# Performance work log

Measured on AMD Instinct MI355X. Metric: run time of the kernel, lower is better.

Reference implementation:

```python
import jax, jax.numpy as jnp
import numpy as np
import math

B, W, BINS, BANDS = 2, 2048, 1024, 8  # cropsize == W
HEAD = BINS // BANDS


def setup_inputs() -> dict:
    key = jax.random.key(0)
    ks = jax.random.split(key, 10)
    s = 1.0 / math.sqrt(BINS)
    return {
        "x": jax.random.normal(ks[0], (B, W, BINS), jnp.float32),
        "Wq": jax.random.normal(ks[1], (BINS, BINS), jnp.float32) * s,
        "bq": jax.random.normal(ks[2], (BINS,), jnp.float32) * s,
        "Wk": jax.random.normal(ks[3], (BINS, BINS), jnp.float32) * s,
        "bk": jax.random.normal(ks[4], (BINS,), jnp.float32) * s,
        "Wv": jax.random.normal(ks[5], (BINS, BINS), jnp.float32) * s,
        "bv": jax.random.normal(ks[6], (BINS,), jnp.float32) * s,
        "Wo": jax.random.normal(ks[7], (BINS, BINS), jnp.float32) * s,
        "bo": jax.random.normal(ks[8], (BINS,), jnp.float32) * s,
        "er": jax.random.normal(ks[9], (HEAD, W), jnp.float32) * s,  # [bins//num_bands, cropsize]
    }


def reference(x, Wq, bq, Wk, bk, Wv, bv, Wo, bo, er):
    b, w, h = x.shape
    n = BANDS
    # projections -> [b, n, w, head]
    q = (x @ Wq.T + bq).reshape(b, w, n, -1).transpose(0, 2, 1, 3)
    k = (x @ Wk.T + bk).reshape(b, w, n, -1).transpose(0, 2, 1, 3)
    v = (x @ Wv.T + bv).reshape(b, w, n, -1).transpose(0, 2, 1, 3)
    # relative position bias via skew trick: [b, n, w, cropsize]
    qer = jnp.einsum('bnwd,dc->bnwc', q, er)
    p = jnp.pad(qer, ((0, 0), (0, 0), (0, 0), (1, 0)))  # pad left of last dim
    p = jnp.swapaxes(p, 2, 3)[:, :, 1:, :]              # [b, n, w, w]
    a = (jnp.einsum('bnqd,bnkd->bnqk', q, k) + p) / math.sqrt(h)
    attn = jax.nn.softmax(a, axis=-1)
    ctx = jnp.einsum('bnqk,bnkd->bnqd', attn, v).transpose(0, 2, 1, 3).reshape(b, w, h)
    o = ctx @ Wo.T + bo
    return (o, a)
```

## Files before the change

kernel.cpp:

```cpp
#include <hip/hip_runtime.h>

typedef __attribute__((ext_vector_type(8))) __bf16 bf16x8;
typedef __attribute__((ext_vector_type(4))) float f32x4;

__device__ __forceinline__ unsigned short f2bf(float f) {
  __bf16 h = (__bf16)f;
  return __builtin_bit_cast(unsigned short, h);
}

__device__ __forceinline__ f32x4 mfma_bf16(bf16x8 a, bf16x8 b, f32x4 c) {
  return __builtin_amdgcn_mfma_f32_16x16x32_bf16(a, b, c, 0, 0, 0);
}

__device__ __forceinline__ void gload_lds16(const void* g, void* l) {
  __builtin_amdgcn_global_load_lds((const __attribute__((address_space(1))) void*)g,
                                   (__attribute__((address_space(3))) void*)l, 16, 0, 0);
}


__global__ void cvt_f32_bf16(const float* __restrict__ in, unsigned short* __restrict__ out, int n4) {
  int i = blockIdx.x * blockDim.x + threadIdx.x;
  if (i < n4) {
    float4 v = reinterpret_cast<const float4*>(in)[i];
    ushort4 o;
    o.x = f2bf(v.x); o.y = f2bf(v.y); o.z = f2bf(v.z); o.w = f2bf(v.w);
    reinterpret_cast<ushort4*>(out)[i] = o;
  }
}

__global__ void cvt4_f32_bf16(const float* __restrict__ a, const float* __restrict__ b,
                              const float* __restrict__ c, const float* __restrict__ d,
                              unsigned short* __restrict__ oa, unsigned short* __restrict__ ob,
                              unsigned short* __restrict__ oc, unsigned short* __restrict__ od) {
  int i = blockIdx.x * blockDim.x + threadIdx.x;
  int which = i >> 18, j = i & 262143;
  const float* src = (which == 0) ? a : (which == 1) ? b : (which == 2) ? c : d;
  unsigned short* dst = (which == 0) ? oa : (which == 1) ? ob : (which == 2) ? oc : od;
  float4 v = reinterpret_cast<const float4*>(src)[j];
  ushort4 o;
  o.x = f2bf(v.x); o.y = f2bf(v.y); o.z = f2bf(v.z); o.w = f2bf(v.w);
  reinterpret_cast<ushort4*>(dst)[j] = o;
}

__global__ void er_transpose(const float* __restrict__ er, unsigned short* __restrict__ ert) {
  __shared__ float t[32][33];
  int w0 = blockIdx.x * 32, d0 = blockIdx.y * 32;
  int tx = threadIdx.x, ty = threadIdx.y;
#pragma unroll
  for (int i = 0; i < 4; ++i)
    t[ty + i * 8][tx] = er[(size_t)(d0 + ty + i * 8) * 2048 + w0 + tx];
  __syncthreads();
#pragma unroll
  for (int i = 0; i < 4; ++i)
    ert[(size_t)(w0 + ty + i * 8) * 128 + d0 + tx] = f2bf(t[tx][ty + i * 8]);
}


__device__ __forceinline__ void gemm_tile(
    const unsigned short* __restrict__ A,
    const unsigned short* __restrict__ Bt,
    const float* __restrict__ bias,
    void* __restrict__ C,
    int mode, int i0, int j0,
    unsigned short* lds)
{
  unsigned short* Al = lds;
  unsigned short* Bl = lds + 4096;

  const int tid = threadIdx.x;
  const int lane = tid & 63, wid = tid >> 6;
  const int lr = lane & 15, lq = lane >> 4;
  const int wr = wid >> 1, wc = wid & 1;

  f32x4 acc[4][4] = {};

  const int srow = tid >> 2;
  const int scolb = (tid & 3) << 4;

  const char* Abase = (const char*)A + (size_t)(i0 + srow) * 2048 + scolb;
  const char* Bbase = (const char*)Bt + (size_t)(j0 + srow) * 2048 + scolb;

  for (int kt = 0; kt < 32; ++kt) {
    const int k0b = kt * 64;
    __syncthreads();
    gload_lds16(Abase + k0b,             (char*)Al + tid * 16);
    gload_lds16(Abase + k0b + 64 * 2048, (char*)Al + 4096 + tid * 16);
    gload_lds16(Bbase + k0b,             (char*)Bl + tid * 16);
    gload_lds16(Bbase + k0b + 64 * 2048, (char*)Bl + 4096 + tid * 16);
    __syncthreads();

    bf16x8 af[4], bfr[4];
#pragma unroll
    for (int m = 0; m < 4; ++m)
      af[m] = *(const bf16x8*)((const char*)Al + (wr * 64 + m * 16 + lr) * 64 + lq * 16);
#pragma unroll
    for (int n = 0; n < 4; ++n)
      bfr[n] = *(const bf16x8*)((const char*)Bl + (wc * 64 + n * 16 + lr) * 64 + lq * 16);
    __builtin_amdgcn_s_setprio(1);
#pragma unroll
    for (int m = 0; m < 4; ++m)
#pragma unroll
      for (int n = 0; n < 4; ++n)
        acc[m][n] = mfma_bf16(af[m], bfr[n], acc[m][n]);
    __builtin_amdgcn_s_setprio(0);
  }

  float bv[4];
#pragma unroll
  for (int n = 0; n < 4; ++n) bv[n] = bias[j0 + wc * 64 + n * 16 + lr];

  if (mode == 1) {
    __syncthreads();
#pragma unroll
    for (int m = 0; m < 4; ++m)
#pragma unroll
      for (int n = 0; n < 4; ++n)
#pragma unroll
        for (int r = 0; r < 4; ++r) {
          int il = wr * 64 + m * 16 + lq * 4 + r;
          int jl = wc * 64 + n * 16 + lr;
          lds[jl * 132 + il] = f2bf(acc[m][n][r] + bv[n]);
        }
    __syncthreads();
    const int b = i0 >> 11, w0 = i0 & 2047, bd = j0 >> 7;
    unsigned short* out = (unsigned short*)C;
    for (int idx = tid; idx < 16384; idx += 256) {
      int dl = idx >> 7, wl = idx & 127;
      out[(size_t)((b * 8 + bd) * 128 + dl) * 2048 + w0 + wl] = lds[dl * 132 + wl];
    }
  } else if (mode == 0) {
    unsigned short* out = (unsigned short*)C;
#pragma unroll
    for (int m = 0; m < 4; ++m)
#pragma unroll
      for (int n = 0; n < 4; ++n)
#pragma unroll
        for (int r = 0; r < 4; ++r) {
          int gi = i0 + wr * 64 + m * 16 + lq * 4 + r;
          int gj = j0 + wc * 64 + n * 16 + lr;
          out[(size_t)gi * 1024 + gj] = f2bf(acc[m][n][r] + bv[n]);
        }
  } else {
    float* out = (float*)C;
#pragma unroll
    for (int m = 0; m < 4; ++m)
#pragma unroll
      for (int n = 0; n < 4; ++n)
#pragma unroll
        for (int r = 0; r < 4; ++r) {
          int gi = i0 + wr * 64 + m * 16 + lq * 4 + r;
          int gj = j0 + wc * 64 + n * 16 + lr;
          out[(size_t)gi * 1024 + gj] = acc[m][n][r] + bv[n];
        }
  }
}

__global__ __launch_bounds__(256, 2) void gemm_qkv(
    const unsigned short* __restrict__ xb,
    const unsigned short* __restrict__ Wqb, const unsigned short* __restrict__ Wkb,
    const unsigned short* __restrict__ Wvb,
    const float* __restrict__ bq, const float* __restrict__ bk, const float* __restrict__ bv_,
    unsigned short* __restrict__ Qb, unsigned short* __restrict__ Kb,
    unsigned short* __restrict__ Vtb)
{
  __shared__ unsigned short lds[16896];
  const int which = blockIdx.y >> 3;
  const int i0 = blockIdx.x * 128, j0 = (blockIdx.y & 7) * 128;
  const unsigned short* Bt = (which == 0) ? Wqb : (which == 1) ? Wkb : Wvb;
  const float* bias = (which == 0) ? bq : (which == 1) ? bk : bv_;
  void* C = (which == 0) ? (void*)Qb : (which == 1) ? (void*)Kb : (void*)Vtb;
  gemm_tile(xb, Bt, bias, C, (which == 2) ? 1 : 0, i0, j0, lds);
}

__global__ __launch_bounds__(256, 2) void gemm_bt(
    const unsigned short* __restrict__ A,
    const unsigned short* __restrict__ Bt,
    const float* __restrict__ bias,
    void* __restrict__ C,
    int mode)
{
  __shared__ unsigned short lds[16896];
  gemm_tile(A, Bt, bias, C, mode, blockIdx.x * 128, blockIdx.y * 128, lds);
}


__global__ __launch_bounds__(512) void attn_fused(
    const unsigned short* __restrict__ Qb,
    const unsigned short* __restrict__ Kb,
    const unsigned short* __restrict__ Vt,
    const unsigned short* __restrict__ ErT,
    float* __restrict__ a_out,
    unsigned short* __restrict__ ctx)
{
  __shared__ __align__(16) char Klb[32768];
  __shared__ __align__(16) char Qlb[32768];
  __shared__ __align__(16) char Vlb[32768];
  __shared__ __align__(16) char Plb[32768];

  const int bb = blockIdx.x;
  const int bd = bb & 7, b = bb >> 3;
  const int qi0 = blockIdx.y * 128;
  const int tid = threadIdx.x, wid = tid >> 6, lane = tid & 63;
  const int lr = lane & 15, lq = lane >> 4;

  bf16x8 qf[4], ef[4];
  {
    const unsigned short* Qrow = Qb + (size_t)(b * 2048 + qi0 + wid * 16 + lr) * 1024 + bd * 128;
    const unsigned short* Erow = ErT + (size_t)(qi0 + wid * 16 + lr) * 128;
#pragma unroll
    for (int kk = 0; kk < 4; ++kk) {
      qf[kk] = *(const bf16x8*)(Qrow + kk * 32 + lq * 8);
      ef[kk] = *(const bf16x8*)(Erow + kk * 32 + lq * 8);
    }
  }

  int ldso[4];
  const char *ksrc[4], *qsrc[4], *vsrc[4];
#pragma unroll
  for (int p = 0; p < 4; ++p) {
    int L = p * 8192 + tid * 16;
    int row = L >> 8, cs = L & 255;
    int sc = cs ^ ((row & 7) << 4);
    ldso[p] = L;
    ksrc[p] = (const char*)Kb + ((size_t)(b * 2048 + row) * 1024 + bd * 128) * 2 + sc;
    qsrc[p] = (const char*)Qb + ((size_t)(b * 2048 + row) * 1024 + bd * 128) * 2 + sc;
    vsrc[p] = (const char*)Vt + ((size_t)(bb * 128 + row) * 2048) * 2 + sc;
  }

#pragma unroll
  for (int p = 0; p < 4; ++p) gload_lds16(ksrc[p], Klb + ldso[p]);
#pragma unroll
  for (int p = 0; p < 4; ++p) gload_lds16(qsrc[p], Qlb + ldso[p]);
#pragma unroll
  for (int p = 0; p < 4; ++p) gload_lds16(vsrc[p], Vlb + ldso[p]);

  f32x4 oacc[8] = {};
  float M[4], L[4];
#pragma unroll
  for (int r = 0; r < 4; ++r) { M[r] = -1e30f; L[r] = 0.f; }

  float* abase = a_out + (size_t)bb * 2048 * 2048;

  for (int kt = 0; kt < 16; ++kt) {
    const int kj0 = kt * 128;
    const size_t nkq = (size_t)((kt + 1) & 15) * 262144;
    const size_t nv = (size_t)((kt + 1) & 15) * 256;

    asm volatile("s_waitcnt vmcnt(4)" ::: "memory");
    __builtin_amdgcn_sched_barrier(0);
    __builtin_amdgcn_s_barrier();
    __builtin_amdgcn_sched_barrier(0);

    f32x4 sacc[8] = {};
    __builtin_amdgcn_s_setprio(1);
#pragma unroll
    for (int kk = 0; kk < 4; ++kk) {
#pragma unroll
      for (int nf = 0; nf < 8; ++nf) {
        const int row = nf * 16 + lr;
        bf16x8 kf = *(const bf16x8*)(Klb + row * 256 + ((kk * 64 + lq * 16) ^ ((row & 7) << 4)));
        sacc[nf] = mfma_bf16(qf[kk], kf, sacc[nf]);
      }
#pragma unroll
      for (int nf = 0; nf < 8; ++nf) {
        const int row = nf * 16 + lr;
        bf16x8 qkf = *(const bf16x8*)(Qlb + row * 256 + ((kk * 64 + lq * 16) ^ ((row & 7) << 4)));
        sacc[nf] = mfma_bf16(ef[kk], qkf, sacc[nf]);
      }
    }
    __builtin_amdgcn_s_setprio(0);

    __builtin_amdgcn_sched_barrier(0);
    __builtin_amdgcn_s_barrier();
    __builtin_amdgcn_sched_barrier(0);

#pragma unroll
    for (int nf = 0; nf < 8; ++nf)
#pragma unroll
      for (int r = 0; r < 4; ++r) sacc[nf][r] *= 0.03125f;
    {
      const int qrow_base = qi0 + wid * 16 + lq * 4;
#pragma unroll
      for (int nf = 0; nf < 8; ++nf)
#pragma unroll
        for (int r = 0; r < 4; ++r)
          abase[(size_t)(qrow_base + r) * 2048 + kj0 + nf * 16 + lr] = sacc[nf][r];
    }

    __builtin_amdgcn_sched_barrier(0);
#pragma unroll
    for (int p = 0; p < 4; ++p) gload_lds16(ksrc[p] + nkq, Klb + ldso[p]);
#pragma unroll
    for (int p = 0; p < 4; ++p) gload_lds16(qsrc[p] + nkq, Qlb + ldso[p]);
    __builtin_amdgcn_sched_barrier(0);

    float rmax[4];
#pragma unroll
    for (int r = 0; r < 4; ++r) {
      float m0 = sacc[0][r];
#pragma unroll
      for (int nf = 1; nf < 8; ++nf) m0 = fmaxf(m0, sacc[nf][r]);
      m0 = fmaxf(m0, __shfl_xor(m0, 1));
      m0 = fmaxf(m0, __shfl_xor(m0, 2));
      m0 = fmaxf(m0, __shfl_xor(m0, 4));
      m0 = fmaxf(m0, __shfl_xor(m0, 8));
      rmax[r] = m0;
    }
    bool small = (rmax[0] - M[0] <= 8.f) & (rmax[1] - M[1] <= 8.f) &
                 (rmax[2] - M[2] <= 8.f) & (rmax[3] - M[3] <= 8.f);
    unsigned long long vote = __ballot(small);
    if (vote != ~0ull) {
      float scl[4];
#pragma unroll
      for (int r = 0; r < 4; ++r) {
        float Mn = fmaxf(M[r], rmax[r]);
        scl[r] = __expf(M[r] - Mn);
        M[r] = Mn;
        L[r] *= scl[r];
      }
#pragma unroll
      for (int dn = 0; dn < 8; ++dn)
#pragma unroll
        for (int r = 0; r < 4; ++r) oacc[dn][r] *= scl[r];
    }
    float rsum[4] = {0.f, 0.f, 0.f, 0.f};
#pragma unroll
    for (int nf = 0; nf < 8; ++nf)
#pragma unroll
      for (int r = 0; r < 4; ++r) {
        float pv = __expf(sacc[nf][r] - M[r]);
        sacc[nf][r] = pv;
        rsum[r] += pv;
      }
    {
      const int prow0 = wid * 16 + lq * 4;
#pragma unroll
      for (int nf = 0; nf < 8; ++nf)
#pragma unroll
        for (int r = 0; r < 4; ++r) {
          const int row = prow0 + r;
          *(unsigned short*)(Plb + row * 256 + (((nf * 16 + lr) * 2) ^ ((row & 7) << 4))) =
              f2bf(sacc[nf][r]);
        }
    }
#pragma unroll
    for (int r = 0; r < 4; ++r) {
      rsum[r] += __shfl_xor(rsum[r], 1);
      rsum[r] += __shfl_xor(rsum[r], 2);
      rsum[r] += __shfl_xor(rsum[r], 4);
      rsum[r] += __shfl_xor(rsum[r], 8);
      L[r] += rsum[r];
    }

    asm volatile("s_waitcnt vmcnt(8)" ::: "memory");
    __builtin_amdgcn_sched_barrier(0);

    __builtin_amdgcn_s_setprio(1);
#pragma unroll
    for (int kk = 0; kk < 4; ++kk) {
      const int prow = wid * 16 + lr;
      bf16x8 pf = *(const bf16x8*)(Plb + prow * 256 + ((kk * 64 + lq * 16) ^ ((prow & 7) << 4)));
#pragma unroll
      for (int dn = 0; dn < 8; ++dn) {
        const int vrow = dn * 16 + lr;
        bf16x8 vf = *(const bf16x8*)(Vlb + vrow * 256 + ((kk * 64 + lq * 16) ^ ((vrow & 7) << 4)));
        oacc[dn] = mfma_bf16(pf, vf, oacc[dn]);
      }
    }
    __builtin_amdgcn_s_setprio(0);

    __builtin_amdgcn_sched_barrier(0);
    __builtin_amdgcn_s_barrier();
    __builtin_amdgcn_sched_barrier(0);
#pragma unroll
    for (int p = 0; p < 4; ++p) gload_lds16(vsrc[p] + nv, Vlb + ldso[p]);
    __builtin_amdgcn_sched_barrier(0);
  }

  {
    const int qrow_base = b * 2048 + qi0 + wid * 16 + lq * 4;
#pragma unroll
    for (int dn = 0; dn < 8; ++dn)
#pragma unroll
      for (int r = 0; r < 4; ++r) {
        float v = oacc[dn][r] / L[r];
        ctx[(size_t)(qrow_base + r) * 1024 + bd * 128 + dn * 16 + lr] = f2bf(v);
      }
  }
}


extern "C" void kernel_launch(void* const* d_in, const int* in_sizes, int n_in,
                              void* d_out, int out_size, void* d_ws, size_t ws_size,
                              hipStream_t stream) {
  const float* x  = (const float*)d_in[0];
  const float* Wq = (const float*)d_in[1];
  const float* bq = (const float*)d_in[2];
  const float* Wk = (const float*)d_in[3];
  const float* bk = (const float*)d_in[4];
  const float* Wv = (const float*)d_in[5];
  const float* bv = (const float*)d_in[6];
  const float* Wo = (const float*)d_in[7];
  const float* bo = (const float*)d_in[8];
  const float* er = (const float*)d_in[9];

  char* ws = (char*)d_ws;
  unsigned short* xb  = (unsigned short*)(ws + 0);
  unsigned short* Wqb = (unsigned short*)(ws + 8388608);
  unsigned short* Wkb = (unsigned short*)(ws + 10485760);
  unsigned short* Wvb = (unsigned short*)(ws + 12582912);
  unsigned short* Wob = (unsigned short*)(ws + 14680064);
  unsigned short* Qb  = (unsigned short*)(ws + 16777216);
  unsigned short* Kb  = (unsigned short*)(ws + 25165824);
  unsigned short* Vtb = (unsigned short*)(ws + 33554432);
  unsigned short* ctx = (unsigned short*)(ws + 41943040);
  unsigned short* ert = (unsigned short*)(ws + 50331648);

  float* a_out = (float*)d_out + 4194304;

  cvt_f32_bf16<<<dim3(4096), dim3(256), 0, stream>>>(x, xb, 1048576);
  cvt4_f32_bf16<<<dim3(4096), dim3(256), 0, stream>>>(Wq, Wk, Wv, Wo, Wqb, Wkb, Wvb, Wob);
  er_transpose<<<dim3(64, 4), dim3(32, 8), 0, stream>>>(er, ert);

  gemm_qkv<<<dim3(32, 24), dim3(256), 0, stream>>>(xb, Wqb, Wkb, Wvb, bq, bk, bv,
                                                   Qb, Kb, Vtb);

  attn_fused<<<dim3(16, 16), dim3(512), 0, stream>>>(Qb, Kb, Vtb, ert, a_out, ctx);

  gemm_bt<<<dim3(32, 8), dim3(256), 0, stream>>>(ctx, Wob, bo, d_out, 2);
}
```

Before: 187.2 us.

## Double-buffer LDS tiles in projection GEMM to overlap loads with MFMA

```diff
diff --git a/kernel.cpp b/kernel.cpp
--- a/kernel.cpp
+++ b/kernel.cpp
@@ -64,8 +64,7 @@
     int mode, int i0, int j0,
     unsigned short* lds)
 {
-  unsigned short* Al = lds;
-  unsigned short* Bl = lds + 4096;
+  char* base = (char*)lds;
 
   const int tid = threadIdx.x;
   const int lane = tid & 63, wid = tid >> 6;
@@ -80,22 +79,36 @@
   const char* Abase = (const char*)A + (size_t)(i0 + srow) * 2048 + scolb;
   const char* Bbase = (const char*)Bt + (size_t)(j0 + srow) * 2048 + scolb;
 
+  gload_lds16(Abase,             base + tid * 16);
+  gload_lds16(Abase + 64 * 2048, base + 4096 + tid * 16);
+  gload_lds16(Bbase,             base + 8192 + tid * 16);
+  gload_lds16(Bbase + 64 * 2048, base + 12288 + tid * 16);
+
   for (int kt = 0; kt < 32; ++kt) {
-    const int k0b = kt * 64;
-    __syncthreads();
-    gload_lds16(Abase + k0b,             (char*)Al + tid * 16);
-    gload_lds16(Abase + k0b + 64 * 2048, (char*)Al + 4096 + tid * 16);
-    gload_lds16(Bbase + k0b,             (char*)Bl + tid * 16);
-    gload_lds16(Bbase + k0b + 64 * 2048, (char*)Bl + 4096 + tid * 16);
-    __syncthreads();
+    char* cbuf = base + (kt & 1) * 16384;
+    char* nbuf = base + ((kt + 1) & 1) * 16384;
+
+    asm volatile("s_waitcnt vmcnt(0)" ::: "memory");
+    __builtin_amdgcn_sched_barrier(0);
+    __builtin_amdgcn_s_barrier();
+    __builtin_amdgcn_sched_barrier(0);
+
+    if (kt < 31) {
+      const int k0b = (kt + 1) * 64;
+      gload_lds16(Abase + k0b,             nbuf + tid * 16);
+      gload_lds16(Abase + k0b + 64 * 2048, nbuf + 4096 + tid * 16);
+      gload_lds16(Bbase + k0b,             nbuf + 8192 + tid * 16);
+      gload_lds16(Bbase + k0b + 64 * 2048, nbuf + 12288 + tid * 16);
+    }
+    __builtin_amdgcn_sched_barrier(0);
 
     bf16x8 af[4], bfr[4];
 #pragma unroll
     for (int m = 0; m < 4; ++m)
-      af[m] = *(const bf16x8*)((const char*)Al + (wr * 64 + m * 16 + lr) * 64 + lq * 16);
+      af[m] = *(const bf16x8*)(cbuf + (wr * 64 + m * 16 + lr) * 64 + lq * 16);
 #pragma unroll
     for (int n = 0; n < 4; ++n)
-      bfr[n] = *(const bf16x8*)((const char*)Bl + (wc * 64 + n * 16 + lr) * 64 + lq * 16);
+      bfr[n] = *(const bf16x8*)(cbuf + 8192 + (wc * 64 + n * 16 + lr) * 64 + lq * 16);
     __builtin_amdgcn_s_setprio(1);
 #pragma unroll
     for (int m = 0; m < 4; ++m)
```

Result: no change. 188.6 us (+0.7%).
